# Kernel tuning notes

Hardware: AMD Instinct MI355X
Metric: run time of the kernel (lower is better)

Reference implementation:

```python
import jax, jax.numpy as jnp
import numpy as np

B, C, H, W = 4, 128, 192, 192

def _conv(x, w, b, pad):
    y = jax.lax.conv_general_dilated(
        x, w, window_strides=(1, 1), padding=[(pad, pad), (pad, pad)],
        dimension_numbers=('NCHW', 'OIHW', 'NCHW'))
    return y + b[None, :, None, None]

def setup_inputs() -> dict:
    key = jax.random.key(0)
    ks = jax.random.split(key, 11)
    def he(k, shape):
        fan_in = shape[1] * shape[2] * shape[3]
        return jax.random.normal(k, shape, jnp.float32) * np.sqrt(2.0 / fan_in)
    return {
        'x':  jax.random.normal(ks[0], (B, C, H, W), jnp.float32),
        'w1': he(ks[1], (C // 2, C, 3, 3)),      'b1': jnp.zeros((C // 2,), jnp.float32),
        'w2': he(ks[2], (C // 4, C // 2, 3, 3)), 'b2': jnp.zeros((C // 4,), jnp.float32),
        'w3': he(ks[3], (9, C // 4, 1, 1)),      'b3': jnp.zeros((9,), jnp.float32),
        'f1': he(ks[4], (C, C, 3, 3)),           'fb1': jnp.zeros((C,), jnp.float32),
        'f2': he(ks[5], (C, C, 3, 3)),           'fb2': jnp.zeros((C,), jnp.float32),
    }

def reference(x, w1, b1, w2, b2, w3, b3, f1, fb1, f2, fb2):
    b, c, h, w = x.shape
    # kernel estimator: conv3x3 -> relu -> conv3x3 -> relu -> conv1x1 (9 logits)
    k = jax.nn.relu(_conv(x, w1, b1, 1))
    k = jax.nn.relu(_conv(k, w2, b2, 1))
    k = _conv(k, w3, b3, 0)                     # (b, 9, h, w)
    kernel = jax.nn.softmax(k, axis=1)[:, None]  # (b, 1, 9, h, w)
    # 3x3 neighborhoods (equivalent to F.unfold with padding=1), row-major taps
    xp = jnp.pad(x, ((0, 0), (0, 0), (1, 1), (1, 1)))
    patches = jnp.stack([xp[:, :, i:i + h, j:j + w]
                         for i in range(3) for j in range(3)], axis=2)  # (b, c, 9, h, w)
    out = jnp.sum(patches * kernel, axis=2)     # (b, c, h, w)
    # feature extract
    feats = jax.nn.relu(_conv(out, f1, fb1, 1))
    feats = _conv(feats, f2, fb2, 1)
    return feats
```

## Files before the change

### kernel.cpp

```cpp
#include <hip/hip_runtime.h>
#include <math.h>

#define BB 4
#define CC 128
#define HH 192
#define WW 192
#define HWSZ (HH * WW)
#define NPIX (BB * HWSZ)
#define PD 194

typedef __attribute__((ext_vector_type(8))) short short8;
typedef __attribute__((ext_vector_type(4))) short short4v;
typedef __attribute__((ext_vector_type(4))) float float4v;

__device__ __forceinline__ short f2bf(float f) {
    unsigned u = __float_as_uint(f);
    u += 0x7FFF + ((u >> 16) & 1);
    return (short)(u >> 16);
}
__device__ __forceinline__ float bf2f(short s) {
    return __uint_as_float(((unsigned)(unsigned short)s) << 16);
}

__global__ void prep_w_kernel(const float* __restrict__ w,
                              short* __restrict__ wp,
                              int CIN, int COUT, int total) {
    int idx = blockIdx.x * blockDim.x + threadIdx.x;
    if (idx >= total) return;
    int ci8 = idx & 7;
    int t   = idx >> 3;
    int co  = t % COUT;  t /= COUT;
    int lg  = t % 4;     t /= 4;
    int tap3 = t % 3;    t /= 3;
    int tt  = t % 3;
    int ck  = t / 3;
    int cin = ck * 32 + lg * 8 + ci8;
    int tap = tt * 3 + tap3;
    wp[idx] = f2bf(w[(co * CIN + cin) * 9 + tap]);
}

__global__ void zero_pads_kernel(short* __restrict__ p0,
                                 short* __restrict__ p1,
                                 short* __restrict__ p2) {
    int idx = blockIdx.x * blockDim.x + threadIdx.x;
    if (idx >= 3 * 64 * 772) return;
    int e   = idx % 772;
    int bc  = (idx / 772) % 64;
    int buf = idx / (772 * 64);
    short* base = (buf == 0) ? p0 : (buf == 1) ? p1 : p2;
    int row, col;
    if (e < 194)      { row = 0;   col = e; }
    else if (e < 388) { row = 193; col = e - 194; }
    else { int e2 = e - 388; row = 1 + (e2 >> 1); col = (e2 & 1) * 193; }
    short8 z = {0, 0, 0, 0, 0, 0, 0, 0};
    *(short8*)&base[(((size_t)bc * PD + row) * PD + col) * 8] = z;
}

__global__ void x_prep_kernel(const float* __restrict__ x,
                              short* __restrict__ xp) {
    int idx = blockIdx.x * blockDim.x + threadIdx.x;
    if (idx >= BB * 16 * HWSZ) return;
    int w  = idx % WW;
    int h  = (idx / WW) % HH;
    int cg = (idx / HWSZ) % 16;
    int b  = idx / (HWSZ * 16);
    const float* p = x + ((size_t)(b * CC + cg * 8) * HH + h) * WW + w;
    short8 pk;
#pragma unroll
    for (int j = 0; j < 8; ++j) pk[j] = f2bf(p[(size_t)j * HWSZ]);
    *(short8*)&xp[((((size_t)b * 16 + cg) * PD + h + 1) * PD + (w + 1)) * 8] = pk;
}

template <int CIN, int COUT, int WAVES_M, int WAVES_N, int WM, int WN,
          bool RELU, bool OUT_F32>
__global__ __launch_bounds__(WAVES_M * WAVES_N * 64, 4)
void conv3x3_wlds(const short* __restrict__ in,
                  const short* __restrict__ wp,
                  const float* __restrict__ bias,
                  void* __restrict__ outv) {
    constexpr int CKN   = CIN / 32;
    constexpr int CG_IN = CIN / 8;
    constexpr int CGO   = COUT / 8;
    constexpr int NT    = WAVES_M * WAVES_N * 64;
    constexpr int SUB   = 3 * 4 * COUT * 8;
    constexpr int NS    = CKN * 3;
    constexpr int KTMAX = CKN * 9;
    static_assert(WAVES_M * WM * 16 == COUT, "M tiling");
    static_assert(WAVES_N * WN * 16 == 192, "N tiling");

    __shared__ __align__(16) short s_w[2 * SUB];

    const int tid  = threadIdx.x;
    const int lin  = blockIdx.y * gridDim.x + blockIdx.x;
    const int L    = (lin & 7) * ((HH * BB) >> 3) + (lin >> 3);
    const int h    = L % HH;
    const int b    = L / HH;
    const int lane = tid & 63;
    const int wv   = tid >> 6;
    const int wv_m = wv % WAVES_M;
    const int wv_n = wv / WAVES_M;
    const int ln15 = lane & 15;
    const int lg   = lane >> 4;

    float4v acc[WM][WN];
#pragma unroll
    for (int mi = 0; mi < WM; ++mi)
#pragma unroll
        for (int ni = 0; ni < WN; ++ni)
            acc[mi][ni] = (float4v){0.f, 0.f, 0.f, 0.f};

    short8 Aa[2][WM], Bb[3][WN];

    auto loadA = [&](int bufp, int tap3, short8* dst) {
#pragma unroll
        for (int mi = 0; mi < WM; ++mi) {
            int co = (wv_m * WM + mi) * 16 + ln15;
            dst[mi] = *(const short8*)
                &s_w[((((bufp * 3 + tap3) * 4 + lg) * COUT) + co) * 8];
        }
    };
    auto loadB = [&](int kt, short8* dst) {
        const int ck = kt / 9, tap = kt % 9;
        const int dy = tap / 3, dx = tap % 3;
#pragma unroll
        for (int ni = 0; ni < WN; ++ni) {
            int col = (wv_n * WN + ni) * 16 + ln15 + dx;
            dst[ni] = *(const short8*)
                &in[((((size_t)b * CG_IN + ck * 4 + lg) * PD + (h + dy)) * PD + col) * 8];
        }
    };
    auto stage = [&](int s) {
        const short* src = wp + (size_t)s * SUB;
        short* dst = &s_w[(s & 1) * SUB];
        constexpr int UNITS = SUB / 8;
#pragma unroll
        for (int u = 0; u < (UNITS + NT - 1) / NT; ++u) {
            int i = tid + u * NT;
            if (UNITS % NT == 0 || i < UNITS)
                __builtin_amdgcn_global_load_lds(
                    (const __attribute__((address_space(1))) void*)&src[i * 8],
                    (__attribute__((address_space(3))) void*)&dst[i * 8], 16, 0, 0);
        }
    };

    loadB(0, Bb[0]);
    loadB(1, Bb[1]);
    stage(0);

    for (int s = 0; s < NS; ++s) {
        __syncthreads();
        if (s + 1 < NS) stage(s + 1);
        const int bufp = s & 1;
        loadA(bufp, 0, Aa[0]);
#pragma unroll
        for (int t3 = 0; t3 < 3; ++t3) {
            const int kt = s * 3 + t3;
            if (t3 < 2) loadA(bufp, t3 + 1, Aa[(t3 + 1) & 1]);
            if (kt + 2 < KTMAX) loadB(kt + 2, Bb[(t3 + 2) % 3]);
#pragma unroll
            for (int mi = 0; mi < WM; ++mi)
#pragma unroll
                for (int ni = 0; ni < WN; ++ni)
                    acc[mi][ni] = __builtin_amdgcn_mfma_f32_16x16x32_bf16(
                        Aa[t3 & 1][mi], Bb[t3 % 3][ni], acc[mi][ni], 0, 0, 0);
        }
    }

    if (OUT_F32) {
        float* out = (float*)outv;
#pragma unroll
        for (int mi = 0; mi < WM; ++mi) {
            int co0 = (wv_m * WM + mi) * 16 + lg * 4;
#pragma unroll
            for (int r = 0; r < 4; ++r) {
                int co = co0 + r;
                float bv = bias[co];
#pragma unroll
                for (int ni = 0; ni < WN; ++ni) {
                    int wcol = (wv_n * WN + ni) * 16 + ln15;
                    float v = acc[mi][ni][r] + bv;
                    if (RELU) v = fmaxf(v, 0.f);
                    out[((size_t)(b * COUT + co) * HH + h) * WW + wcol] = v;
                }
            }
        }
    } else {
        short* out = (short*)outv;
#pragma unroll
        for (int mi = 0; mi < WM; ++mi) {
            int co0 = (wv_m * WM + mi) * 16 + lg * 4;
            int cg  = co0 >> 3;
            int sub = co0 & 7;
#pragma unroll
            for (int ni = 0; ni < WN; ++ni) {
                int wcol = (wv_n * WN + ni) * 16 + ln15;
                short4v pk;
#pragma unroll
                for (int r = 0; r < 4; ++r) {
                    float v = acc[mi][ni][r] + bias[co0 + r];
                    if (RELU) v = fmaxf(v, 0.f);
                    pk[r] = f2bf(v);
                }
                *(short4v*)&out[((((size_t)b * CGO + cg) * PD + (h + 1)) * PD +
                                 (wcol + 1)) * 8 + sub] = pk;
            }
        }
    }
}

__global__ void conv1x1_softmax_kernel(const short* __restrict__ t2,
                                       const float* __restrict__ w3,
                                       const float* __restrict__ b3,
                                       float* __restrict__ kern) {
    __shared__ float sw[9 * 32];
    __shared__ float sb[9];
    for (int i = threadIdx.x; i < 9 * 32; i += blockDim.x) sw[i] = w3[i];
    if (threadIdx.x < 9) sb[threadIdx.x] = b3[threadIdx.x];
    __syncthreads();

    int idx = blockIdx.x * blockDim.x + threadIdx.x;
    if (idx >= NPIX) return;
    int b = idx / HWSZ;
    int p = idx % HWSZ;
    int h = p / WW, w = p % WW;

    float v[32];
#pragma unroll
    for (int cg = 0; cg < 4; ++cg) {
        short8 pk = *(const short8*)
            &t2[((((size_t)b * 4 + cg) * PD + h + 1) * PD + (w + 1)) * 8];
#pragma unroll
        for (int j = 0; j < 8; ++j) v[cg * 8 + j] = bf2f(pk[j]);
    }

    float lg[9];
    float m = -1e30f;
#pragma unroll
    for (int t = 0; t < 9; ++t) {
        float s = sb[t];
#pragma unroll
        for (int c = 0; c < 32; ++c) s = fmaf(sw[t * 32 + c], v[c], s);
        lg[t] = s;
        m = fmaxf(m, s);
    }
    float sum = 0.f;
#pragma unroll
    for (int t = 0; t < 9; ++t) {
        lg[t] = __expf(lg[t] - m);
        sum += lg[t];
    }
    float inv = 1.f / sum;
#pragma unroll
    for (int t = 0; t < 9; ++t)
        kern[((size_t)(b * 9 + t)) * HWSZ + p] = lg[t] * inv;
}

__global__ void deblur_kernel(const float* __restrict__ x,
                              const float* __restrict__ kern,
                              short* __restrict__ t3) {
    int idx = blockIdx.x * blockDim.x + threadIdx.x;
    if (idx >= BB * 16 * HWSZ) return;
    int w  = idx % WW;
    int h  = (idx / WW) % HH;
    int cg = (idx / HWSZ) % 16;
    int b  = idx / (HWSZ * 16);

    const float* kb = kern + (size_t)(b * 9) * HWSZ + h * WW + w;
    float kv[9];
#pragma unroll
    for (int t = 0; t < 9; ++t) kv[t] = kb[(size_t)t * HWSZ];

    const float* xb = x + (size_t)(b * CC + cg * 8) * HWSZ;
    float s[8] = {0.f, 0.f, 0.f, 0.f, 0.f, 0.f, 0.f, 0.f};
    int t = 0;
#pragma unroll
    for (int dy = 0; dy < 3; ++dy) {
#pragma unroll
        for (int dx = 0; dx < 3; ++dx) {
            int hh = h + dy - 1, ww2 = w + dx - 1;
            if ((unsigned)hh < (unsigned)HH && (unsigned)ww2 < (unsigned)WW) {
                const float* xp = xb + hh * WW + ww2;
#pragma unroll
                for (int j = 0; j < 8; ++j)
                    s[j] = fmaf(kv[t], xp[(size_t)j * HWSZ], s[j]);
            }
            ++t;
        }
    }
    short8 pk;
#pragma unroll
    for (int j = 0; j < 8; ++j) pk[j] = f2bf(s[j]);
    *(short8*)&t3[((((size_t)b * 16 + cg) * PD + h + 1) * PD + (w + 1)) * 8] = pk;
}

extern "C" void kernel_launch(void* const* d_in, const int* in_sizes, int n_in,
                              void* d_out, int out_size, void* d_ws, size_t ws_size,
                              hipStream_t stream) {
    const float* x   = (const float*)d_in[0];
    const float* w1  = (const float*)d_in[1];
    const float* b1  = (const float*)d_in[2];
    const float* w2  = (const float*)d_in[3];
    const float* b2  = (const float*)d_in[4];
    const float* w3  = (const float*)d_in[5];
    const float* b3  = (const float*)d_in[6];
    const float* f1  = (const float*)d_in[7];
    const float* fb1 = (const float*)d_in[8];
    const float* f2  = (const float*)d_in[9];
    const float* fb2 = (const float*)d_in[10];
    float* out = (float*)d_out;

    const size_t ACT_SZ = (size_t)BB * 16 * PD * PD * 8;
    short* xpad    = (short*)d_ws;
    short* regionA = xpad + ACT_SZ;
    short* regionB = regionA + ACT_SZ;
    float* kern    = (float*)(regionB + ACT_SZ);
    short* wp1     = (short*)(kern + (size_t)BB * 9 * HWSZ);
    short* wp2     = wp1 + 9 * 4 * 64 * 32;
    short* wpf1    = wp2 + 9 * 2 * 32 * 32;
    short* wpf2    = wpf1 + 9 * 4 * 128 * 32;

    short* t1 = regionA;
    short* t2 = regionB;
    short* t3 = regionA;
    short* t4 = regionB;

    {
        int nz = 3 * 64 * 772;
        zero_pads_kernel<<<(nz + 255) / 256, 256, 0, stream>>>(xpad, regionA, regionB);
        int nx = BB * 16 * HWSZ;
        x_prep_kernel<<<(nx + 255) / 256, 256, 0, stream>>>(x, xpad);
        int n1 = 9 * 4 * 64 * 32, n2 = 9 * 2 * 32 * 32, nf = 9 * 4 * 128 * 32;
        prep_w_kernel<<<(n1 + 255) / 256, 256, 0, stream>>>(w1, wp1, 128, 64, n1);
        prep_w_kernel<<<(n2 + 255) / 256, 256, 0, stream>>>(w2, wp2, 64, 32, n2);
        prep_w_kernel<<<(nf + 255) / 256, 256, 0, stream>>>(f1, wpf1, 128, 128, nf);
        prep_w_kernel<<<(nf + 255) / 256, 256, 0, stream>>>(f2, wpf2, 128, 128, nf);
    }

    conv3x3_wlds<128, 64, 1, 4, 4, 3, true, false>
        <<<dim3(HH, BB), 256, 0, stream>>>(xpad, wp1, b1, t1);
    conv3x3_wlds<64, 32, 1, 4, 2, 3, true, false>
        <<<dim3(HH, BB), 256, 0, stream>>>(t1, wp2, b2, t2);
    conv1x1_softmax_kernel<<<(NPIX + 255) / 256, 256, 0, stream>>>(t2, w3, b3, kern);
    {
        int nd = BB * 16 * HWSZ;
        deblur_kernel<<<(nd + 255) / 256, 256, 0, stream>>>(x, kern, t3);
    }
    conv3x3_wlds<128, 128, 2, 4, 4, 3, true, false>
        <<<dim3(HH, BB), 512, 0, stream>>>(t3, wpf1, fb1, t4);
    conv3x3_wlds<128, 128, 2, 4, 4, 3, false, true>
        <<<dim3(HH, BB), 512, 0, stream>>>(t4, wpf2, fb2, out);
}
```

Baseline: 347.6 us.

## Pipeline conv weight staging with manual vmcnt waits and precomputed input pointers

Rewrites the conv3x3 main loop so the weight tile for the next stage is issued into LDS before computing the current stage. A raw s_barrier guarded by explicit s_waitcnt vmcnt counts replaces __syncthreads, so the wait covers only the weight loads and not the in-flight input prefetches. Input and LDS addresses are precomputed as byte pointers that advance per channel chunk, which removes per-iteration index arithmetic. The hardcoded vmcnt values depend on the exact number of outstanding loads per thread, so a different tiling configuration could break synchronisation.

```diff
diff --git a/kernel.cpp b/kernel.cpp
--- a/kernel.cpp
+++ b/kernel.cpp
@@ -83,8 +83,11 @@
     constexpr int CGO   = COUT / 8;
     constexpr int NT    = WAVES_M * WAVES_N * 64;
     constexpr int SUB   = 3 * 4 * COUT * 8;
+    constexpr int SUBB  = SUB * 2;
+    constexpr int ATS   = 4 * COUT * 16;
     constexpr int NS    = CKN * 3;
     constexpr int KTMAX = CKN * 9;
+    constexpr int CKB   = PD * PD * 64;
     static_assert(WAVES_M * WM * 16 == COUT, "M tiling");
     static_assert(WAVES_N * WN * 16 == 192, "N tiling");
 
@@ -111,58 +114,87 @@
 
     short8 Aa[2][WM], Bb[3][WN];
 
-    auto loadA = [&](int bufp, int tap3, short8* dst) {
-#pragma unroll
-        for (int mi = 0; mi < WM; ++mi) {
-            int co = (wv_m * WM + mi) * 16 + ln15;
-            dst[mi] = *(const short8*)
-                &s_w[((((bufp * 3 + tap3) * 4 + lg) * COUT) + co) * 8];
-        }
+    const int colb = (wv_n * WN * 16 + ln15) * 16;
+    const char* rowb0 = (const char*)(in +
+        (((size_t)b * CG_IN + lg) * PD + h) * (size_t)PD * 8) + colb;
+    const char* rowb1 = rowb0 + PD * 16;
+    const char* rowb2 = rowb0 + 2 * PD * 16;
+
+    const char* aBase = (const char*)&s_w[0] +
+        lg * (COUT * 16) + (wv_m * WM) * 256 + ln15 * 16;
+
+    auto loadBpf = [&](int dy, int dx, short8* dst) {
+        const char* rp = (dy == 0) ? rowb0 : (dy == 1) ? rowb1 : rowb2;
+#pragma unroll
+        for (int ni = 0; ni < WN; ++ni)
+            dst[ni] = *(const short8*)(rp + dx * 16 + ni * 256);
     };
-    auto loadB = [&](int kt, short8* dst) {
-        const int ck = kt / 9, tap = kt % 9;
-        const int dy = tap / 3, dx = tap % 3;
-#pragma unroll
-        for (int ni = 0; ni < WN; ++ni) {
-            int col = (wv_n * WN + ni) * 16 + ln15 + dx;
-            dst[ni] = *(const short8*)
-                &in[((((size_t)b * CG_IN + ck * 4 + lg) * PD + (h + dy)) * PD + col) * 8];
-        }
-    };
-    auto stage = [&](int s) {
-        const short* src = wp + (size_t)s * SUB;
-        short* dst = &s_w[(s & 1) * SUB];
+
+    const short* wsrc = wp;
+    int wpar = 0;
+    auto stageIssue = [&]() {
         constexpr int UNITS = SUB / 8;
+        short* dstb = &s_w[wpar * SUB];
 #pragma unroll
         for (int u = 0; u < (UNITS + NT - 1) / NT; ++u) {
             int i = tid + u * NT;
             if (UNITS % NT == 0 || i < UNITS)
                 __builtin_amdgcn_global_load_lds(
-                    (const __attribute__((address_space(1))) void*)&src[i * 8],
-                    (__attribute__((address_space(3))) void*)&dst[i * 8], 16, 0, 0);
-        }
+                    (const __attribute__((address_space(1))) void*)&wsrc[i * 8],
+                    (__attribute__((address_space(3))) void*)&dstb[i * 8], 16, 0, 0);
+        }
+        asm volatile("" ::: "memory");
+        wsrc += SUB;
+        wpar ^= 1;
     };
 
-    loadB(0, Bb[0]);
-    loadB(1, Bb[1]);
-    stage(0);
-
-    for (int s = 0; s < NS; ++s) {
-        __syncthreads();
-        if (s + 1 < NS) stage(s + 1);
-        const int bufp = s & 1;
-        loadA(bufp, 0, Aa[0]);
-#pragma unroll
-        for (int t3 = 0; t3 < 3; ++t3) {
-            const int kt = s * 3 + t3;
-            if (t3 < 2) loadA(bufp, t3 + 1, Aa[(t3 + 1) & 1]);
-            if (kt + 2 < KTMAX) loadB(kt + 2, Bb[(t3 + 2) % 3]);
+    stageIssue();
+    loadBpf(0, 0, Bb[0]);
+    loadBpf(0, 1, Bb[1]);
+    asm volatile("s_waitcnt vmcnt(6)" ::: "memory");
+    __builtin_amdgcn_s_barrier();
+    asm volatile("" ::: "memory");
+
+    int par = 0;
+    for (int ck = 0; ck < CKN; ++ck) {
+#pragma unroll
+        for (int tt = 0; tt < 3; ++tt) {
+            const int s = ck * 3 + tt;
+            const bool notLast = (s + 1 < NS);
+            if (notLast) stageIssue();
+            const char* aP = aBase + (par ? SUBB : 0);
 #pragma unroll
             for (int mi = 0; mi < WM; ++mi)
-#pragma unroll
-                for (int ni = 0; ni < WN; ++ni)
-                    acc[mi][ni] = __builtin_amdgcn_mfma_f32_16x16x32_bf16(
-                        Aa[t3 & 1][mi], Bb[t3 % 3][ni], acc[mi][ni], 0, 0, 0);
+                Aa[0][mi] = *(const short8*)(aP + mi * 256);
+#pragma unroll
+            for (int t3 = 0; t3 < 3; ++t3) {
+                if (t3 < 2) {
+#pragma unroll
+                    for (int mi = 0; mi < WM; ++mi)
+                        Aa[(t3 + 1) & 1][mi] =
+                            *(const short8*)(aP + (t3 + 1) * ATS + mi * 256);
+                }
+                const int kt = s * 3 + t3;
+                if (kt + 2 < KTMAX) {
+                    const int tp = (tt * 3 + t3 + 2) % 9;
+                    loadBpf(tp / 3, tp % 3, Bb[(t3 + 2) % 3]);
+                }
+#pragma unroll
+                for (int mi = 0; mi < WM; ++mi)
+#pragma unroll
+                    for (int ni = 0; ni < WN; ++ni)
+                        acc[mi][ni] = __builtin_amdgcn_mfma_f32_16x16x32_bf16(
+                            Aa[t3 & 1][mi], Bb[t3][ni], acc[mi][ni], 0, 0, 0);
+                if (tt == 2 && t3 == 0) {
+                    rowb0 += CKB; rowb1 += CKB; rowb2 += CKB;
+                }
+            }
+            if (notLast) {
+                asm volatile("s_waitcnt vmcnt(9)" ::: "memory");
+                __builtin_amdgcn_s_barrier();
+                asm volatile("" ::: "memory");
+                par ^= 1;
+            }
         }
     }
 
```

After: 349.2 us. No clear change (+0.4%).
